# Optimization experiments

Hardware: AMD Instinct MI355X
Metric: run time of the kernel (lower is better)

The kernel has to match this reference:

```python
import jax, jax.numpy as jnp
import numpy as np
import math

EPS = 1e-3          # self.eps
M = 0.5             # margin
H = 0.333           # rad_h
S = 64.0            # scale
HEAD_B = 0.5        # head_b
BATCH_MEAN = 0.0    # registered buffer initial value
BATCH_STD = 100.0   # registered buffer initial value
B, D, C = 1024, 512, 51332


def setup_inputs() -> dict:
    key = jax.random.key(0)
    k1, k2, k3, k4 = jax.random.split(key, 4)
    emb = jax.random.normal(k1, (B, D), dtype=jnp.float32)
    # face embeddings are typically l2-normalized before this head
    emb = emb / jnp.clip(jnp.linalg.norm(emb, axis=1, keepdims=True), 1e-5)
    # feature norms in a realistic range [5, 35)
    norms = jax.random.uniform(k2, (B, 1), dtype=jnp.float32) * 30.0 + 5.0
    kernel = jax.random.normal(k3, (D, C), dtype=jnp.float32)
    label = jax.random.randint(k4, (B,), 0, C)
    return {"embbedings": emb, "norms": norms, "kernel": kernel, "label": label}


def reference(embbedings, norms, kernel, label):
    # l2_norm(kernel, axis=0)
    kn = kernel / jnp.clip(jnp.linalg.norm(kernel, axis=0, keepdims=True), 1e-5)
    # [B, C] cosine logits
    cosine = jnp.clip(embbedings @ kn, -1.0 + EPS, 1.0 - EPS)
    # detached norm-based margin scaler ('batchnorm' branch)
    safe_norms = jax.lax.stop_gradient(jnp.clip(norms, 1e-3, 100.0))
    ms = jnp.clip((safe_norms - BATCH_MEAN) / (BATCH_STD + EPS) * H, -1.0, 1.0)[:, 0]  # [B]
    rows = jnp.arange(cosine.shape[0])
    # additive angular margin only at the label column (equivalent to the one-hot scatter)
    theta = jnp.arccos(cosine).at[rows, label].add(M * ms)
    cos_m = jnp.cos(jnp.clip(theta, EPS, math.pi - EPS))
    # subtractive cosine margin at the label column
    cos_m = cos_m.at[rows, label].add(-(HEAD_B - M * ms))
    return cos_m * S
```

## Files before the change

kernel.cpp:

```cpp
#include <hip/hip_runtime.h>
#include <hip/hip_bf16.h>
#include <math.h>

#define B_ROWS 1024
#define DDIM   512
#define CN     51332
#define CPAD   51456
#define EPSF   1e-3f
#define SCALE  64.0f

typedef unsigned short ushort_t;
typedef short bf16x8 __attribute__((ext_vector_type(8)));
typedef float f32x4  __attribute__((ext_vector_type(4)));
typedef unsigned short us8 __attribute__((ext_vector_type(8)));
typedef unsigned short us4 __attribute__((ext_vector_type(4)));

static __device__ __forceinline__ unsigned short f2bf(float f) {
    unsigned int u = __float_as_uint(f);
    u += 0x7fffu + ((u >> 16) & 1u);
    return (unsigned short)(u >> 16);
}

__global__ void colpass(const float* __restrict__ kern, ushort_t* __restrict__ kbT,
                        float* __restrict__ partials) {
    const int c  = blockIdx.x * 256 + threadIdx.x;
    const int dc = blockIdx.y;
    const int d0 = dc * 128;
    const bool valid = (c < CN);
    float s = 0.f;
    for (int d = d0; d < d0 + 128; d += 8) {
        us8 pk;
#pragma unroll
        for (int j = 0; j < 8; ++j) {
            float v = valid ? kern[(size_t)(d + j) * CN + c] : 0.f;
            s += v * v;
            pk[j] = f2bf(v);
        }
        *(us8*)&kbT[(size_t)c * DDIM + d] = pk;
    }
    partials[(size_t)dc * CPAD + c] = s;
}

__global__ void finnorm(const float* __restrict__ partials, float* __restrict__ inv_norm) {
    const int c = blockIdx.x * 256 + threadIdx.x;
    float s = partials[c] + partials[CPAD + c] + partials[2 * CPAD + c] + partials[3 * CPAD + c];
    inv_norm[c] = 1.0f / fmaxf(sqrtf(s), 1e-5f);
}

__global__ void embcast(const float* __restrict__ emb, ushort_t* __restrict__ embb) {
    const int t = blockIdx.x * 256 + threadIdx.x;
    const float4 v = ((const float4*)emb)[t];
    us4 o; o[0] = f2bf(v.x); o[1] = f2bf(v.y); o[2] = f2bf(v.z); o[3] = f2bf(v.w);
    *(us4*)&embb[(size_t)t * 4] = o;
}

__global__ __launch_bounds__(256) void gemm_kernel(
        const ushort_t* __restrict__ embb, const ushort_t* __restrict__ kbT,
        const float* __restrict__ inv_norm, float* __restrict__ out) {
    __shared__ ushort_t smem[2 * 128 * 64];
    ushort_t* As = smem;
    ushort_t* Bs = smem + 128 * 64;
    float*    Es = (float*)smem;

    const int bid = blockIdx.x;
    const int u   = (bid & 7) * 402 + (bid >> 3);
    const int m0  = (u & 7) * 128;
    const int n0  = (u >> 3) * 128;

    const int tid  = threadIdx.x;
    const int lane = tid & 63;
    const int wave = tid >> 6;
    const int wm = wave & 1, wn = wave >> 1;
    const int r8 = lane >> 3, c8 = lane & 7;
    const int lm = lane & 15;
    const int lq = lane >> 4;

    f32x4 acc[4][4];
#pragma unroll
    for (int i = 0; i < 4; ++i)
#pragma unroll
        for (int j = 0; j < 4; ++j)
            acc[i][j] = (f32x4){0.f, 0.f, 0.f, 0.f};

    for (int kt = 0; kt < 8; ++kt) {
        const int k0 = kt * 64;
#pragma unroll
        for (int it = 0; it < 4; ++it) {
            const int row = wave * 32 + it * 8;
            const ushort_t* gA = embb + (size_t)(m0 + row + r8) * DDIM + k0 + c8 * 8;
            __builtin_amdgcn_global_load_lds((__attribute__((address_space(1))) void*)gA,
                (__attribute__((address_space(3))) void*)&As[row * 64], 16, 0, 0);
            const ushort_t* gB = kbT + (size_t)(n0 + row + r8) * DDIM + k0 + c8 * 8;
            __builtin_amdgcn_global_load_lds((__attribute__((address_space(1))) void*)gB,
                (__attribute__((address_space(3))) void*)&Bs[row * 64], 16, 0, 0);
        }
        __syncthreads();
#pragma unroll
        for (int ks = 0; ks < 64; ks += 32) {
            bf16x8 a[4], b[4];
#pragma unroll
            for (int i = 0; i < 4; ++i)
                a[i] = *(const bf16x8*)&As[(wm * 64 + i * 16 + lm) * 64 + ks + lq * 8];
#pragma unroll
            for (int j = 0; j < 4; ++j)
                b[j] = *(const bf16x8*)&Bs[(wn * 64 + j * 16 + lm) * 64 + ks + lq * 8];
#pragma unroll
            for (int i = 0; i < 4; ++i)
#pragma unroll
                for (int j = 0; j < 4; ++j)
                    acc[i][j] = __builtin_amdgcn_mfma_f32_16x16x32_bf16(a[i], b[j], acc[i][j], 0, 0, 0);
        }
        __syncthreads();
    }

    float invn[4];
#pragma unroll
    for (int j = 0; j < 4; ++j) {
        const int col = n0 + wn * 64 + j * 16 + lm;
        invn[j] = (col < CN) ? inv_norm[col] : 0.f;
    }

#pragma unroll
    for (int half = 0; half < 2; ++half) {
        __syncthreads();
        if (wm == half) {
#pragma unroll
            for (int i = 0; i < 4; ++i)
#pragma unroll
                for (int j = 0; j < 4; ++j)
#pragma unroll
                    for (int r = 0; r < 4; ++r) {
                        const int row = i * 16 + lq * 4 + r;
                        const int col = wn * 64 + j * 16 + lm;
                        const int cs  = (col + row * 4) & 127;
                        float v = acc[i][j][r] * invn[j];
                        v = fminf(fmaxf(v, -(1.0f - EPSF)), 1.0f - EPSF) * SCALE;
                        Es[row * 128 + cs] = v;
                    }
        }
        __syncthreads();
#pragma unroll
        for (int it = 0; it < 8; ++it) {
            const int row = wave * 16 + it * 2 + (lane >> 5);
            const int uq  = lane & 31;
            const int us_ = (uq + row) & 31;
            const f32x4 v = *(const f32x4*)&Es[row * 128 + us_ * 4];
            const int grow = m0 + half * 64 + row;
            const int gcol = n0 + uq * 4;
            float* p = &out[(size_t)grow * CN + gcol];
            if (gcol + 3 < CN) {
                *(f32x4*)p = v;
            } else {
#pragma unroll
                for (int e = 0; e < 4; ++e)
                    if (gcol + e < CN) p[e] = v[e];
            }
        }
    }
}

__global__ void fixup(const float* __restrict__ norms, const int* __restrict__ label,
                      float* __restrict__ out) {
    const int b = blockIdx.x * 256 + threadIdx.x;
    if (b >= B_ROWS) return;
    const int c = label[b];
    const float safe = fminf(fmaxf(norms[b], 1e-3f), 100.0f);
    const float ms = fminf(fmaxf(safe / (100.0f + 1e-3f) * 0.333f, -1.0f), 1.0f);
    const size_t idx = (size_t)b * CN + c;
    const float cosv = out[idx] * (1.0f / SCALE);
    float theta = acosf(cosv) + 0.5f * ms;
    theta = fminf(fmaxf(theta, EPSF), 3.14159265358979f - EPSF);
    out[idx] = (cosf(theta) - (0.5f - 0.5f * ms)) * SCALE;
}

extern "C" void kernel_launch(void* const* d_in, const int* in_sizes, int n_in,
                              void* d_out, int out_size, void* d_ws, size_t ws_size,
                              hipStream_t stream) {
    const float* emb   = (const float*)d_in[0];
    const float* norms = (const float*)d_in[1];
    const float* kern  = (const float*)d_in[2];
    const int*   label = (const int*)d_in[3];
    float* out = (float*)d_out;

    char* ws = (char*)d_ws;
    ushort_t* kbT = (ushort_t*)ws;
    size_t off = (size_t)CPAD * DDIM * 2;
    ushort_t* embb = (ushort_t*)(ws + off); off += (size_t)B_ROWS * DDIM * 2;
    float* inv_norm = (float*)(ws + off);   off += (size_t)CPAD * 4;
    float* partials = (float*)(ws + off);

    colpass<<<dim3(CPAD / 256, 4), 256, 0, stream>>>(kern, kbT, partials);
    embcast<<<dim3((B_ROWS * DDIM / 4) / 256), 256, 0, stream>>>(emb, embb);
    finnorm<<<dim3(CPAD / 256), 256, 0, stream>>>(partials, inv_norm);
    gemm_kernel<<<dim3(3216), 256, 0, stream>>>(embb, kbT, inv_norm, out);
    fixup<<<dim3(B_ROWS / 256), 256, 0, stream>>>(norms, label, out);
}
```

Measured before the change: 457.7 us.

## Rewrite GEMM as 256x256 tile with 8 waves, swizzled LDS and ping-pong pipeline

The cosine GEMM moves from 128x128 tiles with 4 waves to 256x256 tiles with 8 waves per block. It uses XOR-swizzled LDS staging and double-buffered A/B loads that are issued between MFMA phases, with barriers and setprio so memory and compute overlap. The epilogue now stages the output through per-wave LDS buffers and writes 16-byte vectors. The column-norm pass handles two columns per thread with float2 loads and splits D into eight chunks instead of four. This aims to raise MFMA use and data reuse, at the cost of much higher register and LDS pressure and fragile hand-written waitcnt and barrier choreography.

Result: faster. 431.1 us (-5.8%).

```diff
diff --git a/kernel.cpp b/kernel.cpp
--- a/kernel.cpp
+++ b/kernel.cpp
@@ -8,6 +8,7 @@
 #define CPAD   51456
 #define EPSF   1e-3f
 #define SCALE  64.0f
+#define NT     8
 
 typedef unsigned short ushort_t;
 typedef short bf16x8 __attribute__((ext_vector_type(8)));
@@ -23,27 +24,35 @@
 
 __global__ void colpass(const float* __restrict__ kern, ushort_t* __restrict__ kbT,
                         float* __restrict__ partials) {
-    const int c  = blockIdx.x * 256 + threadIdx.x;
-    const int dc = blockIdx.y;
-    const int d0 = dc * 128;
-    const bool valid = (c < CN);
-    float s = 0.f;
-    for (int d = d0; d < d0 + 128; d += 8) {
-        us8 pk;
+    const int c2 = (blockIdx.x * 256 + threadIdx.x) * 2;
+    if (c2 >= CPAD) return;
+    const int d0 = blockIdx.y * 64;
+    const bool valid = (c2 < CN);
+    float s0 = 0.f, s1 = 0.f;
+    for (int d = d0; d < d0 + 64; d += 8) {
+        us8 p0, p1;
 #pragma unroll
         for (int j = 0; j < 8; ++j) {
-            float v = valid ? kern[(size_t)(d + j) * CN + c] : 0.f;
-            s += v * v;
-            pk[j] = f2bf(v);
-        }
-        *(us8*)&kbT[(size_t)c * DDIM + d] = pk;
-    }
-    partials[(size_t)dc * CPAD + c] = s;
+            float x = 0.f, y = 0.f;
+            if (valid) {
+                const float2 v = *(const float2*)&kern[(size_t)(d + j) * CN + c2];
+                x = v.x; y = v.y;
+            }
+            s0 += x * x; s1 += y * y;
+            p0[j] = f2bf(x); p1[j] = f2bf(y);
+        }
+        *(us8*)&kbT[(size_t)c2 * DDIM + d]       = p0;
+        *(us8*)&kbT[(size_t)(c2 + 1) * DDIM + d] = p1;
+    }
+    partials[(size_t)blockIdx.y * CPAD + c2]     = s0;
+    partials[(size_t)blockIdx.y * CPAD + c2 + 1] = s1;
 }
 
 __global__ void finnorm(const float* __restrict__ partials, float* __restrict__ inv_norm) {
     const int c = blockIdx.x * 256 + threadIdx.x;
-    float s = partials[c] + partials[CPAD + c] + partials[2 * CPAD + c] + partials[3 * CPAD + c];
+    float s = 0.f;
+#pragma unroll
+    for (int k = 0; k < 8; ++k) s += partials[(size_t)k * CPAD + c];
     inv_norm[c] = 1.0f / fmaxf(sqrtf(s), 1e-5f);
 }
 
@@ -54,64 +63,143 @@
     *(us4*)&embb[(size_t)t * 4] = o;
 }
 
-__global__ __launch_bounds__(256) void gemm_kernel(
+#define MFMA(d, va, vb) (d) = __builtin_amdgcn_mfma_f32_16x16x32_bf16((va), (vb), (d), 0, 0, 0)
+
+#define STAGE16(gp, lp) __builtin_amdgcn_global_load_lds( \
+    (__attribute__((address_space(1))) void*)(gp), \
+    (__attribute__((address_space(3))) void*)(lp), 16, 0, 0)
+
+#define STAGE(gl, sb, half, kstep) do { \
+    const int rb_ = (half) * 128 + w * 16; \
+    STAGE16((gl) + (size_t)rb_ * DDIM + (size_t)(kstep) * 64, &(sb)[rb_ * 64]); \
+    STAGE16((gl) + (size_t)(rb_ + 8) * DDIM + (size_t)(kstep) * 64, &(sb)[(rb_ + 8) * 64]); \
+} while (0)
+
+__global__ __launch_bounds__(512, 2) void gemm_kernel(
         const ushort_t* __restrict__ embb, const ushort_t* __restrict__ kbT,
         const float* __restrict__ inv_norm, float* __restrict__ out) {
-    __shared__ ushort_t smem[2 * 128 * 64];
-    ushort_t* As = smem;
-    ushort_t* Bs = smem + 128 * 64;
-    float*    Es = (float*)smem;
-
-    const int bid = blockIdx.x;
-    const int u   = (bid & 7) * 402 + (bid >> 3);
-    const int m0  = (u & 7) * 128;
-    const int n0  = (u >> 3) * 128;
+    __shared__ ushort_t smem[65536];
 
     const int tid  = threadIdx.x;
     const int lane = tid & 63;
-    const int wave = tid >> 6;
-    const int wm = wave & 1, wn = wave >> 1;
+    const int w    = tid >> 6;
+    const int wm = w >> 2, wn = w & 3;
+    const int lm = lane & 15, lq = lane >> 4;
     const int r8 = lane >> 3, c8 = lane & 7;
-    const int lm = lane & 15;
-    const int lq = lane >> 4;
-
-    f32x4 acc[4][4];
-#pragma unroll
-    for (int i = 0; i < 4; ++i)
-#pragma unroll
-        for (int j = 0; j < 4; ++j)
-            acc[i][j] = (f32x4){0.f, 0.f, 0.f, 0.f};
-
-    for (int kt = 0; kt < 8; ++kt) {
-        const int k0 = kt * 64;
-#pragma unroll
-        for (int it = 0; it < 4; ++it) {
-            const int row = wave * 32 + it * 8;
-            const ushort_t* gA = embb + (size_t)(m0 + row + r8) * DDIM + k0 + c8 * 8;
-            __builtin_amdgcn_global_load_lds((__attribute__((address_space(1))) void*)gA,
-                (__attribute__((address_space(3))) void*)&As[row * 64], 16, 0, 0);
-            const ushort_t* gB = kbT + (size_t)(n0 + row + r8) * DDIM + k0 + c8 * 8;
-            __builtin_amdgcn_global_load_lds((__attribute__((address_space(1))) void*)gB,
-                (__attribute__((address_space(3))) void*)&Bs[row * 64], 16, 0, 0);
-        }
-        __syncthreads();
-#pragma unroll
-        for (int ks = 0; ks < 64; ks += 32) {
-            bf16x8 a[4], b[4];
-#pragma unroll
-            for (int i = 0; i < 4; ++i)
-                a[i] = *(const bf16x8*)&As[(wm * 64 + i * 16 + lm) * 64 + ks + lq * 8];
-#pragma unroll
-            for (int j = 0; j < 4; ++j)
-                b[j] = *(const bf16x8*)&Bs[(wn * 64 + j * 16 + lm) * 64 + ks + lq * 8];
-#pragma unroll
-            for (int i = 0; i < 4; ++i)
-#pragma unroll
-                for (int j = 0; j < 4; ++j)
-                    acc[i][j] = __builtin_amdgcn_mfma_f32_16x16x32_bf16(a[i], b[j], acc[i][j], 0, 0, 0);
-        }
-        __syncthreads();
-    }
+
+    const int bid = blockIdx.x;
+    const int xcd = bid & 7, loc = bid >> 3;
+    const int u  = (xcd < 4) ? (xcd * 101 + loc) : (404 + (xcd - 4) * 100 + loc);
+    const int m0 = (u & 3) * 256;
+    const int n0 = (u >> 2) * 256;
+
+    const ushort_t* gAl = embb + (size_t)(m0 + r8) * DDIM + ((c8 ^ r8) << 3);
+    const ushort_t* gBl = kbT  + (size_t)(n0 + r8) * DDIM + ((c8 ^ r8) << 3);
+    const int swz = lm & 7;
+    const int ca0 = ((lq    ) ^ swz) << 3;
+    const int ca1 = ((lq + 4) ^ swz) << 3;
+    const int offA = (wm * 128 + lm) * 64;
+    const int offB = (wn * 64  + lm) * 64;
+
+    f32x4 acc[8][4];
+#pragma unroll
+    for (int i = 0; i < 8; ++i)
+#pragma unroll
+        for (int j = 0; j < 4; ++j) acc[i][j] = (f32x4){0.f, 0.f, 0.f, 0.f};
+
+    STAGE(gAl, (smem        ), 0, 0); STAGE(gAl, (smem        ), 1, 0);
+    STAGE(gBl, (smem + 32768), 0, 0); STAGE(gBl, (smem + 32768), 1, 0);
+    STAGE(gAl, (smem + 16384), 0, 1); STAGE(gAl, (smem + 16384), 1, 1);
+    STAGE(gBl, (smem + 49152), 0, 1);
+    asm volatile("s_waitcnt vmcnt(6)" ::: "memory");
+    __builtin_amdgcn_s_barrier();
+    __builtin_amdgcn_sched_barrier(0);
+
+    bf16x8 a[8][2], b0[2][2], b1[2][2];
+
+    for (int t = 0; t < NT; ++t) {
+        const int cur = t & 1;
+        ushort_t* Sa = smem + cur * 16384;
+        ushort_t* Sb = smem + 32768 + cur * 16384;
+        ushort_t* Nb = smem + 32768 + (cur ^ 1) * 16384;
+        const int kA = (t + 2) & 7;
+        const int kB = (t + 1) & 7;
+
+#pragma unroll
+        for (int i = 0; i < 8; ++i) {
+            a[i][0] = *(const bf16x8*)&Sa[offA + i * 1024 + ca0];
+            a[i][1] = *(const bf16x8*)&Sa[offA + i * 1024 + ca1];
+        }
+#pragma unroll
+        for (int j = 0; j < 2; ++j) {
+            b0[j][0] = *(const bf16x8*)&Sb[offB + j * 1024 + ca0];
+            b0[j][1] = *(const bf16x8*)&Sb[offB + j * 1024 + ca1];
+        }
+        STAGE(gBl, Nb, 1, kB);
+        __builtin_amdgcn_s_barrier();
+        __builtin_amdgcn_s_setprio(1);
+#pragma unroll
+        for (int i = 0; i < 4; ++i)
+#pragma unroll
+            for (int j = 0; j < 2; ++j) {
+                MFMA(acc[i][j], a[i][0], b0[j][0]);
+                MFMA(acc[i][j], a[i][1], b0[j][1]);
+            }
+        __builtin_amdgcn_s_setprio(0);
+        __builtin_amdgcn_s_barrier();
+        __builtin_amdgcn_sched_barrier(0);
+
+#pragma unroll
+        for (int j = 0; j < 2; ++j) {
+            b1[j][0] = *(const bf16x8*)&Sb[offB + (j + 2) * 1024 + ca0];
+            b1[j][1] = *(const bf16x8*)&Sb[offB + (j + 2) * 1024 + ca1];
+        }
+        STAGE(gAl, Sa, 0, kA);
+        __builtin_amdgcn_s_barrier();
+        __builtin_amdgcn_s_setprio(1);
+#pragma unroll
+        for (int i = 0; i < 4; ++i)
+#pragma unroll
+            for (int j = 0; j < 2; ++j) {
+                MFMA(acc[i][j + 2], a[i][0], b1[j][0]);
+                MFMA(acc[i][j + 2], a[i][1], b1[j][1]);
+            }
+        __builtin_amdgcn_s_setprio(0);
+        __builtin_amdgcn_s_barrier();
+        __builtin_amdgcn_sched_barrier(0);
+
+        STAGE(gAl, Sa, 1, kA);
+        __builtin_amdgcn_s_barrier();
+        __builtin_amdgcn_s_setprio(1);
+#pragma unroll
+        for (int i = 4; i < 8; ++i)
+#pragma unroll
+            for (int j = 0; j < 2; ++j) {
+                MFMA(acc[i][j], a[i][0], b0[j][0]);
+                MFMA(acc[i][j], a[i][1], b0[j][1]);
+            }
+        __builtin_amdgcn_s_setprio(0);
+        __builtin_amdgcn_s_barrier();
+        __builtin_amdgcn_sched_barrier(0);
+
+        STAGE(gBl, Sb, 0, kA);
+        __builtin_amdgcn_s_barrier();
+        __builtin_amdgcn_s_setprio(1);
+#pragma unroll
+        for (int i = 4; i < 8; ++i)
+#pragma unroll
+            for (int j = 0; j < 2; ++j) {
+                MFMA(acc[i][j + 2], a[i][0], b1[j][0]);
+                MFMA(acc[i][j + 2], a[i][1], b1[j][1]);
+            }
+        __builtin_amdgcn_s_setprio(0);
+        asm volatile("s_waitcnt vmcnt(6)" ::: "memory");
+        __builtin_amdgcn_s_barrier();
+        __builtin_amdgcn_sched_barrier(0);
+    }
+
+    asm volatile("s_waitcnt vmcnt(0)" ::: "memory");
+    __syncthreads();
 
     float invn[4];
 #pragma unroll
@@ -119,42 +207,28 @@
         const int col = n0 + wn * 64 + j * 16 + lm;
         invn[j] = (col < CN) ? inv_norm[col] : 0.f;
     }
-
-#pragma unroll
-    for (int half = 0; half < 2; ++half) {
-        __syncthreads();
-        if (wm == half) {
-#pragma unroll
-            for (int i = 0; i < 4; ++i)
-#pragma unroll
-                for (int j = 0; j < 4; ++j)
-#pragma unroll
-                    for (int r = 0; r < 4; ++r) {
-                        const int row = i * 16 + lq * 4 + r;
-                        const int col = wn * 64 + j * 16 + lm;
-                        const int cs  = (col + row * 4) & 127;
-                        float v = acc[i][j][r] * invn[j];
-                        v = fminf(fmaxf(v, -(1.0f - EPSF)), 1.0f - EPSF) * SCALE;
-                        Es[row * 128 + cs] = v;
-                    }
-        }
-        __syncthreads();
-#pragma unroll
-        for (int it = 0; it < 8; ++it) {
-            const int row = wave * 16 + it * 2 + (lane >> 5);
-            const int uq  = lane & 31;
-            const int us_ = (uq + row) & 31;
-            const f32x4 v = *(const f32x4*)&Es[row * 128 + us_ * 4];
-            const int grow = m0 + half * 64 + row;
-            const int gcol = n0 + uq * 4;
-            float* p = &out[(size_t)grow * CN + gcol];
-            if (gcol + 3 < CN) {
-                *(f32x4*)p = v;
-            } else {
-#pragma unroll
-                for (int e = 0; e < 4; ++e)
-                    if (gcol + e < CN) p[e] = v[e];
-            }
+    float* Ew = (float*)smem + w * 1024;
+    const int rr = lane >> 4, cc = lane & 15;
+#pragma unroll
+    for (int i = 0; i < 8; ++i) {
+#pragma unroll
+        for (int j = 0; j < 4; ++j)
+#pragma unroll
+            for (int r = 0; r < 4; ++r) {
+                const int row = lq * 4 + r;
+                const int cs  = ((j * 16 + lm) + row * 4) & 63;
+                float v = acc[i][j][r] * invn[j];
+                v = fminf(fmaxf(v, -(1.0f - EPSF)), 1.0f - EPSF) * SCALE;
+                Ew[row * 64 + cs] = v;
+            }
+#pragma unroll
+        for (int rep = 0; rep < 4; ++rep) {
+            const int row = rep * 4 + rr;
+            const f32x4 v = *(const f32x4*)&Ew[row * 64 + ((cc + row) & 15) * 4];
+            const int grow = m0 + wm * 128 + i * 16 + row;
+            const int gcol = n0 + wn * 64 + cc * 4;
+            if (gcol < CN)
+                *(f32x4*)&out[(size_t)grow * CN + gcol] = v;
         }
     }
 }
@@ -189,9 +263,9 @@
     float* inv_norm = (float*)(ws + off);   off += (size_t)CPAD * 4;
     float* partials = (float*)(ws + off);
 
-    colpass<<<dim3(CPAD / 256, 4), 256, 0, stream>>>(kern, kbT, partials);
+    colpass<<<dim3((CPAD / 2 + 255) / 256, 8), 256, 0, stream>>>(kern, kbT, partials);
     embcast<<<dim3((B_ROWS * DDIM / 4) / 256), 256, 0, stream>>>(emb, embb);
     finnorm<<<dim3(CPAD / 256), 256, 0, stream>>>(partials, inv_norm);
-    gemm_kernel<<<dim3(3216), 256, 0, stream>>>(embb, kbT, inv_norm, out);
+    gemm_kernel<<<dim3(804), 512, 0, stream>>>(embb, kbT, inv_norm, out);
     fixup<<<dim3(B_ROWS / 256), 256, 0, stream>>>(norms, label, out);
 }
```
